# Optimization experiments

Hardware: AMD Instinct MI355X
Metric: run time of the kernel (lower is better)

## Reference

```python
import jax, jax.numpy as jnp
import numpy as np

NC = 512  # n_clusters (symbol alphabet size)
# (kernel, stride, padding) for each of the 17 symbolic conv layers
CFGS = [(7, 4, 0), (3, 1, 1), (3, 1, 1), (3, 1, 1), (3, 1, 1), (3, 2, 1),
        (3, 1, 1), (3, 1, 1), (3, 1, 1), (3, 2, 1), (3, 1, 1), (3, 1, 1),
        (3, 1, 1), (3, 2, 1), (3, 1, 1), (3, 1, 1), (3, 1, 1)]
RELU_AFTER = {0, 1, 3, 5, 7, 9, 11, 13, 15}
INS = [3, 64, 64, 64, 64, 64, 128, 128, 128, 128, 256, 256, 256, 256, 512, 512, 512]
OUTS = [64, 64, 64, 64, 64, 128, 128, 128, 128, 256, 256, 256, 256, 512, 512, 512, 512]


def setup_inputs() -> dict:
    key = jax.random.key(0)
    ks = jax.random.split(key, 26)
    inp = {"x": jax.random.normal(ks[0], (8, 3, 67, 67), dtype=jnp.float32)}
    for i in range(17):
        k = CFGS[i][0]
        inp[f"w{i}"] = jax.random.randint(ks[1 + i], (k * k * INS[i], OUTS[i]), 0, NC, dtype=jnp.int32)
    inp["conv_lut"] = jax.random.randint(ks[18], (NC, NC), 0, NC, dtype=jnp.int32)
    inp["add_lut"] = jax.random.randint(ks[19], (NC, NC), 0, NC, dtype=jnp.int32)
    inp["relu_lut"] = jax.random.randint(ks[20], (NC,), 0, NC, dtype=jnp.int32)
    inp["centroid_lut"] = jnp.sort(jax.random.normal(ks[21], (NC,), dtype=jnp.float32))
    inp["fc_w"] = jax.random.normal(ks[22], (1000, 512), dtype=jnp.float32) * 0.02
    inp["fc_b"] = jnp.zeros((1000,), dtype=jnp.float32)
    return inp


def _extract_patches(s, k, st):
    H, W, C = s.shape
    oh = (H - k) // st + 1
    ow = (W - k) // st + 1
    ri = (jnp.arange(oh) * st)[:, None] + jnp.arange(k)[None, :]  # (oh, k)
    ci = (jnp.arange(ow) * st)[:, None] + jnp.arange(k)[None, :]  # (ow, k)
    p = s[ri][:, :, ci]                      # (oh, k, ow, k, C)
    p = p.transpose(0, 2, 1, 3, 4)           # (oh, ow, k, k, C)
    return p.reshape(oh * ow, k * k * C), oh, ow


def _sym_conv(s, W, conv_lut, add_lut, k, st, pad):
    # LUT-based symbolic convolution: gather product symbols then fold the
    # window with the (non-associative) add_lut, exactly like functools.reduce.
    if pad:
        s = jnp.pad(s, ((pad, pad), (pad, pad), (0, 0)))
    pat, oh, ow = _extract_patches(s, k, st)
    m = conv_lut[pat[:, :, None], W[None, :, :]]
    def step(carry, row):                              # sequential LUT reduce over syms
        return add_lut[carry, row], None
    out, _ = jax.lax.scan(step, m[:, 0, :], jnp.moveaxis(m[:, 1:, :], 1, 0))
    return out.reshape(oh, ow, -1)


def reference(x, w0, w1, w2, w3, w4, w5, w6, w7, w8, w9, w10, w11, w12, w13,
              w14, w15, w16, conv_lut, add_lut, relu_lut, centroid_lut, fc_w, fc_b):
    ws = [w0, w1, w2, w3, w4, w5, w6, w7, w8, w9, w10, w11, w12, w13, w14, w15, w16]

    def per_image(img):                                 # img: (3, 67, 67)
        p = img.transpose(1, 2, 0)                      # (67, 67, 3)
        # discretize: nearest-centroid symbol per scalar (patch_size = 1x1)
        s = jnp.argmin((p[..., None] - centroid_lut) ** 2, axis=-1).astype(jnp.int32)
        for i, (k, st, pad) in enumerate(CFGS):
            s = _sym_conv(s, ws[i], conv_lut, add_lut, k, st, pad)
            if i in RELU_AFTER:
                s = relu_lut[s]
        vals = centroid_lut[s]                          # symbolic_to_image: (2, 2, 512)
        return jnp.mean(vals, axis=(0, 1))              # AdaptiveAvgPool2d((1,1)) -> (512,)

    feats = jax.vmap(per_image)(x)                      # (B, 512)
    return feats @ fc_w.T + fc_b                        # classifier: (B, 1000)
```

## Files before the change

### kernel.cpp

```cpp
#include <hip/hip_runtime.h>

typedef unsigned short u16;

#define NSYM 512

__global__ void build_tables_kernel(const int* __restrict__ conv_i,
                                    const int* __restrict__ add_i,
                                    const int* __restrict__ relu_i,
                                    u16* __restrict__ conv_u,
                                    u16* __restrict__ add_u,
                                    u16* __restrict__ addrelu_u) {
    int i = blockIdx.x * blockDim.x + threadIdx.x;
    if (i < NSYM * NSYM) {
        conv_u[i] = (u16)conv_i[i];
        int a = add_i[i];
        add_u[i] = (u16)a;
        addrelu_u[i] = (u16)relu_i[a];
    }
}

__global__ void quantize_kernel(const float* __restrict__ x,
                                u16* __restrict__ s0,
                                const float* __restrict__ cent,
                                int n) {
    __shared__ float c[NSYM];
    for (int t = threadIdx.x; t < NSYM; t += blockDim.x) c[t] = cent[t];
    __syncthreads();
    int i = blockIdx.x * blockDim.x + threadIdx.x;
    if (i >= n) return;
    int ch = i % 3; int t2 = i / 3; int xx = t2 % 67; int t3 = t2 / 67;
    int y = t3 % 67; int img = t3 / 67;
    float v = x[((img * 3 + ch) * 67 + y) * 67 + xx];
    int lo = 0, hi = NSYM;
    while (lo < hi) { int mid = (lo + hi) >> 1; if (c[mid] < v) lo = mid + 1; else hi = mid; }
    int idx;
    if (lo == 0) idx = 0;
    else if (lo == NSYM) idx = NSYM - 1;
    else {
        float d1 = v - c[lo - 1];
        float d2 = v - c[lo];
        idx = (d1 * d1 <= d2 * d2) ? (lo - 1) : lo;
    }
    s0[i] = (u16)idx;
}

__global__ __launch_bounds__(64) void symconv_kernel(
                               const u16* __restrict__ in, u16* __restrict__ out,
                               const int* __restrict__ Wl,
                               const u16* __restrict__ conv,
                               const u16* __restrict__ addt,
                               const u16* __restrict__ addlast,
                               int H, int Wd, int C, int OC, int nOCG,
                               int K, int ST, int PAD, int OH, int OW) {
    extern __shared__ u16 patch[];
    int bid = blockIdx.x;
    int ocg = bid % nOCG;
    int pix = bid / nOCG;
    int img = pix / (OH * OW);
    int rem = pix - img * (OH * OW);
    int oy = rem / OW;
    int ox = rem - oy * OW;
    int J = K * K * C;
    for (int t = threadIdx.x; t < J; t += 64) {
        int c = t % C; int tt = t / C; int kc = tt % K; int kr = tt / K;
        int iy = oy * ST + kr - PAD;
        int ix = ox * ST + kc - PAD;
        u16 v = 0;
        if (iy >= 0 && iy < H && ix >= 0 && ix < Wd)
            v = in[((img * H + iy) * Wd + ix) * C + c];
        patch[t] = v;
    }
    __syncthreads();
    int oc = ocg * 64 + threadIdx.x;

#define GM(j) ((int)conv[((int)patch[(j)] << 9) + Wl[(j) * OC + oc]])

    int carry = GM(0);
    int mA = GM(1);
    int mB = GM(2);
    int mC = GM(3);
    for (int j = 1; j < J - 3; ++j) {
        int mcur = mA; mA = mB; mB = mC;
        mC = GM(j + 3);
        carry = (int)addt[(carry << 9) + mcur];
    }
    carry = (int)addt[(carry << 9) + mA];
    carry = (int)addt[(carry << 9) + mB];
    carry = (int)addlast[(carry << 9) + mC];
    out[pix * OC + oc] = (u16)carry;
#undef GM
}

__global__ void head_kernel(const u16* __restrict__ s,
                            const float* __restrict__ cent,
                            const float* __restrict__ fcw,
                            const float* __restrict__ fcb,
                            float* __restrict__ out) {
    __shared__ float feats[NSYM];
    int img = blockIdx.x;
    const u16* sp = s + img * 4 * NSYM;
    for (int c = threadIdx.x; c < NSYM; c += blockDim.x) {
        float acc = cent[sp[c]] + cent[sp[NSYM + c]] +
                    cent[sp[2 * NSYM + c]] + cent[sp[3 * NSYM + c]];
        feats[c] = acc * 0.25f;
    }
    __syncthreads();
    int o = blockIdx.y * blockDim.x + threadIdx.x;
    if (o < 1000) {
        float acc = fcb[o];
        const float* wr = fcw + o * NSYM;
        for (int c2 = 0; c2 < NSYM; ++c2) acc += feats[c2] * wr[c2];
        out[img * 1000 + o] = acc;
    }
}

extern "C" void kernel_launch(void* const* d_in, const int* in_sizes, int n_in,
                              void* d_out, int out_size, void* d_ws, size_t ws_size,
                              hipStream_t stream) {
    const float* x = (const float*)d_in[0];
    const int* w[17];
    for (int i = 0; i < 17; ++i) w[i] = (const int*)d_in[1 + i];
    const int* conv_i = (const int*)d_in[18];
    const int* add_i  = (const int*)d_in[19];
    const int* relu_i = (const int*)d_in[20];
    const float* cent = (const float*)d_in[21];
    const float* fcw  = (const float*)d_in[22];
    const float* fcb  = (const float*)d_in[23];
    float* out = (float*)d_out;

    char* p = (char*)d_ws;
    u16* conv_u    = (u16*)p; p += NSYM * NSYM * 2;
    u16* add_u     = (u16*)p; p += NSYM * NSYM * 2;
    u16* addrelu_u = (u16*)p; p += NSYM * NSYM * 2;
    u16* act0      = (u16*)p; p += ((8 * 67 * 67 * 3 * 2 + 255) / 256) * 256;
    u16* actA      = (u16*)p; p += 8 * 16 * 16 * 64 * 2;
    u16* actB      = (u16*)p; p += 8 * 16 * 16 * 64 * 2;

    build_tables_kernel<<<(NSYM * NSYM + 255) / 256, 256, 0, stream>>>(
        conv_i, add_i, relu_i, conv_u, add_u, addrelu_u);

    int nq = 8 * 67 * 67 * 3;
    quantize_kernel<<<(nq + 255) / 256, 256, 0, stream>>>(x, act0, cent, nq);

    struct LC { int K, ST, PAD, C, OC, H, OH, relu; };
    static const LC L[17] = {
        {7,4,0,  3, 64,67,16,1},
        {3,1,1, 64, 64,16,16,1},
        {3,1,1, 64, 64,16,16,0},
        {3,1,1, 64, 64,16,16,1},
        {3,1,1, 64, 64,16,16,0},
        {3,2,1, 64,128,16, 8,1},
        {3,1,1,128,128, 8, 8,0},
        {3,1,1,128,128, 8, 8,1},
        {3,1,1,128,128, 8, 8,0},
        {3,2,1,128,256, 8, 4,1},
        {3,1,1,256,256, 4, 4,0},
        {3,1,1,256,256, 4, 4,1},
        {3,1,1,256,256, 4, 4,0},
        {3,2,1,256,512, 4, 2,1},
        {3,1,1,512,512, 2, 2,0},
        {3,1,1,512,512, 2, 2,1},
        {3,1,1,512,512, 2, 2,0},
    };

    const u16* cur = act0;
    u16* nxt = actA;
    for (int i = 0; i < 17; ++i) {
        int OH = L[i].OH, OW = L[i].OH;
        int nOCG = L[i].OC / 64;
        int grid = 8 * OH * OW * nOCG;
        int J = L[i].K * L[i].K * L[i].C;
        symconv_kernel<<<grid, 64, J * 2, stream>>>(
            cur, nxt, w[i], conv_u, add_u, L[i].relu ? addrelu_u : add_u,
            L[i].H, L[i].H, L[i].C, L[i].OC, nOCG,
            L[i].K, L[i].ST, L[i].PAD, OH, OW);
        cur = nxt;
        nxt = (nxt == actA) ? actB : actA;
    }

    head_kernel<<<dim3(8, 4), 256, 0, stream>>>(cur, cent, fcw, fcb, out);
}
```

Measured before the change: 6.376 ms.

## Split symconv into producer and consumer waves with double-buffered LDS chunks

Each block now runs two waves. One wave gathers conv-LUT product symbols for the next chunk of the window into a swizzled LDS buffer, while the other wave runs the serial add-LUT fold over the current chunk. The aim is to hide the gather latency (weight load plus conv table lookup) behind the dependent add chain. This costs twice the threads per block, extra LDS per block, and a block-wide barrier after every chunk.

```diff
diff --git a/kernel.cpp b/kernel.cpp
--- a/kernel.cpp
+++ b/kernel.cpp
@@ -1,6 +1,7 @@
 #include <hip/hip_runtime.h>
 
 typedef unsigned short u16;
+typedef __attribute__((ext_vector_type(8))) short short8;
 
 #define NSYM 512
 
@@ -44,15 +45,21 @@
     s0[i] = (u16)idx;
 }
 
-__global__ __launch_bounds__(64) void symconv_kernel(
-                               const u16* __restrict__ in, u16* __restrict__ out,
-                               const int* __restrict__ Wl,
-                               const u16* __restrict__ conv,
-                               const u16* __restrict__ addt,
-                               const u16* __restrict__ addlast,
-                               int H, int Wd, int C, int OC, int nOCG,
-                               int K, int ST, int PAD, int OH, int OW) {
-    extern __shared__ u16 patch[];
+__global__ __launch_bounds__(128) void symconv_kernel(
+        const u16* __restrict__ in, u16* __restrict__ out,
+        const int* __restrict__ Wl,
+        const u16* __restrict__ conv,
+        const u16* __restrict__ addt,
+        const u16* __restrict__ addlast,
+        int H, int Wd, int C, int OC, int nOCG,
+        int K, int ST, int PAD, int OH, int OW, int CH) {
+    extern __shared__ char lds[];
+    int J = K * K * C;
+    u16* patch = (u16*)lds;
+    int patchBytes = (J * 2 + 127) & ~127;
+    char* mbuf0 = lds + patchBytes;
+    char* mbuf1 = mbuf0 + CH * 64 * 2;
+
     int bid = blockIdx.x;
     int ocg = bid % nOCG;
     int pix = bid / nOCG;
@@ -60,8 +67,8 @@
     int rem = pix - img * (OH * OW);
     int oy = rem / OW;
     int ox = rem - oy * OW;
-    int J = K * K * C;
-    for (int t = threadIdx.x; t < J; t += 64) {
+
+    for (int t = threadIdx.x; t < J; t += 128) {
         int c = t % C; int tt = t / C; int kc = tt % K; int kr = tt / K;
         int iy = oy * ST + kr - PAD;
         int ix = ox * ST + kc - PAD;
@@ -71,24 +78,95 @@
         patch[t] = v;
     }
     __syncthreads();
-    int oc = ocg * 64 + threadIdx.x;
-
-#define GM(j) ((int)conv[((int)patch[(j)] << 9) + Wl[(j) * OC + oc]])
-
-    int carry = GM(0);
-    int mA = GM(1);
-    int mB = GM(2);
-    int mC = GM(3);
-    for (int j = 1; j < J - 3; ++j) {
-        int mcur = mA; mA = mB; mB = mC;
-        mC = GM(j + 3);
-        carry = (int)addt[(carry << 9) + mcur];
-    }
-    carry = (int)addt[(carry << 9) + mA];
-    carry = (int)addt[(carry << 9) + mB];
-    carry = (int)addlast[(carry << 9) + mC];
-    out[pix * OC + oc] = (u16)carry;
-#undef GM
+
+    int wave = threadIdx.x >> 6;
+    int lane = threadIdx.x & 63;
+    int oc = ocg * 64 + lane;
+    int nch = (J + CH - 1) / CH;
+    int rowbase = lane * CH * 2;
+    int lsw = lane & 7;
+
+    auto produce = [&](int t) {
+        char* dst = (t & 1) ? mbuf1 : mbuf0;
+        int j0 = t * CH;
+        int n = min(CH, J - j0);
+        int nfull = n >> 3, tail = n & 7;
+        for (int g = 0; g < nfull; ++g) {
+            u16 v[8];
+            #pragma unroll
+            for (int u = 0; u < 8; ++u) {
+                int j = j0 + g * 8 + u;
+                int wv = Wl[j * OC + oc];
+                v[u] = conv[((int)patch[j] << 9) + wv];
+            }
+            short8 pk;
+            #pragma unroll
+            for (int u = 0; u < 8; ++u) pk[u] = (short)v[u];
+            *(short8*)(dst + rowbase + ((g ^ lsw) << 4)) = pk;
+        }
+        for (int u = 0; u < tail; ++u) {
+            int j = j0 + nfull * 8 + u;
+            int wv = Wl[j * OC + oc];
+            u16 vv = conv[((int)patch[j] << 9) + wv];
+            *(u16*)(dst + rowbase + ((nfull ^ lsw) << 4) + (u << 1)) = vv;
+        }
+    };
+
+    int carry = 0;
+
+    auto chain = [&](int t) {
+        const char* src = (t & 1) ? mbuf1 : mbuf0;
+        int j0 = t * CH;
+        int n = min(CH, J - j0);
+        bool lastchunk = (j0 + n == J);
+        int ncha = n - (lastchunk ? 1 : 0);
+        int nfull = ncha >> 3, tail = ncha & 7;
+        short8 cur, nxt;
+        int g = 0;
+        if (nfull > 0) {
+            cur = *(const short8*)(src + rowbase + ((0 ^ lsw) << 4));
+            if (t == 0) {
+                if (nfull > 1) nxt = *(const short8*)(src + rowbase + ((1 ^ lsw) << 4));
+                carry = (int)(unsigned short)cur[0];
+                #pragma unroll
+                for (int u = 1; u < 8; ++u)
+                    carry = (int)addt[(carry << 9) + (int)(unsigned short)cur[u]];
+                cur = nxt;
+                g = 1;
+            }
+        }
+        for (; g < nfull; ++g) {
+            if (g + 1 < nfull)
+                nxt = *(const short8*)(src + rowbase + (((g + 1) ^ lsw) << 4));
+            #pragma unroll
+            for (int u = 0; u < 8; ++u)
+                carry = (int)addt[(carry << 9) + (int)(unsigned short)cur[u]];
+            cur = nxt;
+        }
+        for (int u = 0; u < tail; ++u) {
+            int jj = nfull * 8 + u;
+            int m = (int)*(const u16*)(src + rowbase + (((jj >> 3) ^ lsw) << 4) + ((jj & 7) << 1));
+            if (t == 0 && jj == 0) carry = m;
+            else carry = (int)addt[(carry << 9) + m];
+        }
+        if (lastchunk) {
+            int jj = n - 1;
+            int m = (int)*(const u16*)(src + rowbase + (((jj >> 3) ^ lsw) << 4) + ((jj & 7) << 1));
+            carry = (int)addlast[(carry << 9) + m];
+        }
+    };
+
+    if (wave == 1) produce(0);
+    __syncthreads();
+    for (int t = 0; t < nch; ++t) {
+        if (wave == 1) {
+            if (t + 1 < nch) produce(t + 1);
+        } else {
+            chain(t);
+        }
+        __syncthreads();
+    }
+    if (wave == 0) out[pix * OC + oc] = (u16)carry;
 }
 
 __global__ void head_kernel(const u16* __restrict__ s,
@@ -162,6 +240,8 @@
         {3,1,1,512,512, 2, 2,1},
         {3,1,1,512,512, 2, 2,0},
     };
+    static const int CHs[17] = {64, 64,64,64,64, 128, 128,128,128,
+                                192, 192,192,192, 192, 192,192,192};
 
     const u16* cur = act0;
     u16* nxt = actA;
@@ -170,10 +250,13 @@
         int nOCG = L[i].OC / 64;
         int grid = 8 * OH * OW * nOCG;
         int J = L[i].K * L[i].K * L[i].C;
-        symconv_kernel<<<grid, 64, J * 2, stream>>>(
+        int CH = CHs[i];
+        int patchBytes = (J * 2 + 127) & ~127;
+        int ldsBytes = patchBytes + CH * 256;
+        symconv_kernel<<<grid, 128, ldsBytes, stream>>>(
             cur, nxt, w[i], conv_u, add_u, L[i].relu ? addrelu_u : add_u,
             L[i].H, L[i].H, L[i].C, L[i].OC, nOCG,
-            L[i].K, L[i].ST, L[i].PAD, OH, OW);
+            L[i].K, L[i].ST, L[i].PAD, OH, OW, CH);
         cur = nxt;
         nxt = (nxt == actA) ? actB : actA;
     }
```

New measurement: 6.499 ms. About the same (+1.9%).

## Stage weight slice in LDS and share it across several pixels per block

Applied to the files above, without the earlier changes.

Adds a kernel variant that loads the 64-output-channel weight slice for a layer into shared memory as u16, then runs PPB waves, one pixel each, that reuse it. The goal is to cut repeated global int32 weight loads, which the old one-pixel-per-block kernel issued per pixel. Early layers (up to layer 9) use the new path and deeper layers keep the original per-pixel kernel. The cost is much larger LDS use per block (up to about 147KB for layer 9), which lowers occupancy, and a raised dynamic shared memory limit.

```diff
diff --git a/kernel.cpp b/kernel.cpp
--- a/kernel.cpp
+++ b/kernel.cpp
@@ -44,14 +44,76 @@
     s0[i] = (u16)idx;
 }
 
-__global__ __launch_bounds__(64) void symconv_kernel(
-                               const u16* __restrict__ in, u16* __restrict__ out,
-                               const int* __restrict__ Wl,
-                               const u16* __restrict__ conv,
-                               const u16* __restrict__ addt,
-                               const u16* __restrict__ addlast,
-                               int H, int Wd, int C, int OC, int nOCG,
-                               int K, int ST, int PAD, int OH, int OW) {
+__global__ __launch_bounds__(512) void symconv_ldsw_kernel(
+        const u16* __restrict__ in, u16* __restrict__ out,
+        const int* __restrict__ Wl,
+        const u16* __restrict__ conv,
+        const u16* __restrict__ addt,
+        const u16* __restrict__ addlast,
+        int H, int C, int OC, int nOCG,
+        int K, int ST, int PAD, int OH, int OW, int PPB) {
+    extern __shared__ u16 lds[];
+    int J = K * K * C;
+    u16* wlds = lds;
+    u16* patch = lds + J * 64;
+
+    int bid = blockIdx.x;
+    int ocg = bid % nOCG;
+    int pblk = bid / nOCG;
+    int pixel0 = pblk * PPB;
+    int tid = threadIdx.x;
+    int nthr = PPB << 6;
+
+    for (int t = tid; t < J * 64; t += nthr) {
+        int j = t >> 6; int ocp = t & 63;
+        wlds[t] = (u16)Wl[j * OC + (ocg << 6) + ocp];
+    }
+    for (int t = tid; t < PPB * J; t += nthr) {
+        int p = t / J; int j = t - p * J;
+        int c = j % C; int tt = j / C; int kc = tt % K; int kr = tt / K;
+        int pix = pixel0 + p;
+        int img = pix / (OH * OW); int rem = pix - img * (OH * OW);
+        int oy = rem / OW; int ox = rem - oy * OW;
+        int iy = oy * ST + kr - PAD;
+        int ix = ox * ST + kc - PAD;
+        u16 v = 0;
+        if (iy >= 0 && iy < H && ix >= 0 && ix < H)
+            v = in[((img * H + iy) * H + ix) * C + c];
+        patch[p * J + j] = v;
+    }
+    __syncthreads();
+
+    int wave = tid >> 6;
+    int lane = tid & 63;
+    int pix = pixel0 + wave;
+    const u16* pat = patch + wave * J;
+
+#define GM(j) ((int)conv[((int)pat[(j)] << 9) + (int)wlds[((j) << 6) + lane]])
+
+    int carry = GM(0);
+    int mA = GM(1);
+    int mB = GM(2);
+    int mC = GM(3);
+    for (int j = 1; j < J - 3; ++j) {
+        int mcur = mA; mA = mB; mB = mC;
+        mC = GM(j + 3);
+        carry = (int)addt[(carry << 9) + mcur];
+    }
+    carry = (int)addt[(carry << 9) + mA];
+    carry = (int)addt[(carry << 9) + mB];
+    carry = (int)addlast[(carry << 9) + mC];
+    out[pix * OC + (ocg << 6) + lane] = (u16)carry;
+#undef GM
+}
+
+__global__ __launch_bounds__(64) void symconv_glob_kernel(
+        const u16* __restrict__ in, u16* __restrict__ out,
+        const int* __restrict__ Wl,
+        const u16* __restrict__ conv,
+        const u16* __restrict__ addt,
+        const u16* __restrict__ addlast,
+        int H, int C, int OC, int nOCG,
+        int K, int ST, int PAD, int OH, int OW) {
     extern __shared__ u16 patch[];
     int bid = blockIdx.x;
     int ocg = bid % nOCG;
@@ -66,12 +128,12 @@
         int iy = oy * ST + kr - PAD;
         int ix = ox * ST + kc - PAD;
         u16 v = 0;
-        if (iy >= 0 && iy < H && ix >= 0 && ix < Wd)
-            v = in[((img * H + iy) * Wd + ix) * C + c];
+        if (iy >= 0 && iy < H && ix >= 0 && ix < H)
+            v = in[((img * H + iy) * H + ix) * C + c];
         patch[t] = v;
     }
     __syncthreads();
-    int oc = ocg * 64 + threadIdx.x;
+    int oc = (ocg << 6) + threadIdx.x;
 
 #define GM(j) ((int)conv[((int)patch[(j)] << 9) + Wl[(j) * OC + oc]])
 
@@ -142,38 +204,61 @@
     int nq = 8 * 67 * 67 * 3;
     quantize_kernel<<<(nq + 255) / 256, 256, 0, stream>>>(x, act0, cent, nq);
 
-    struct LC { int K, ST, PAD, C, OC, H, OH, relu; };
+    struct LC { int K, ST, PAD, C, OC, H, OH, relu, PPB; };
     static const LC L[17] = {
-        {7,4,0,  3, 64,67,16,1},
-        {3,1,1, 64, 64,16,16,1},
-        {3,1,1, 64, 64,16,16,0},
-        {3,1,1, 64, 64,16,16,1},
-        {3,1,1, 64, 64,16,16,0},
-        {3,2,1, 64,128,16, 8,1},
-        {3,1,1,128,128, 8, 8,0},
-        {3,1,1,128,128, 8, 8,1},
-        {3,1,1,128,128, 8, 8,0},
-        {3,2,1,128,256, 8, 4,1},
-        {3,1,1,256,256, 4, 4,0},
-        {3,1,1,256,256, 4, 4,1},
-        {3,1,1,256,256, 4, 4,0},
-        {3,2,1,256,512, 4, 2,1},
-        {3,1,1,512,512, 2, 2,0},
-        {3,1,1,512,512, 2, 2,1},
-        {3,1,1,512,512, 2, 2,0},
+        {7,4,0,  3, 64,67,16,1, 8},
+        {3,1,1, 64, 64,16,16,1, 8},
+        {3,1,1, 64, 64,16,16,0, 8},
+        {3,1,1, 64, 64,16,16,1, 8},
+        {3,1,1, 64, 64,16,16,0, 8},
+        {3,2,1, 64,128,16, 8,1, 4},
+        {3,1,1,128,128, 8, 8,0, 4},
+        {3,1,1,128,128, 8, 8,1, 4},
+        {3,1,1,128,128, 8, 8,0, 4},
+        {3,2,1,128,256, 8, 4,1, 2},
+        {3,1,1,256,256, 4, 4,0, 0},
+        {3,1,1,256,256, 4, 4,1, 0},
+        {3,1,1,256,256, 4, 4,0, 0},
+        {3,2,1,256,512, 4, 2,1, 0},
+        {3,1,1,512,512, 2, 2,0, 0},
+        {3,1,1,512,512, 2, 2,1, 0},
+        {3,1,1,512,512, 2, 2,0, 0},
     };
+
+    int maxlds = 0;
+    for (int i = 0; i < 17; ++i) {
+        if (L[i].PPB > 0) {
+            int J = L[i].K * L[i].K * L[i].C;
+            int b = J * 64 * 2 + L[i].PPB * J * 2;
+            if (b > maxlds) maxlds = b;
+        }
+    }
+    hipFuncSetAttribute((const void*)symconv_ldsw_kernel,
+                        hipFuncAttributeMaxDynamicSharedMemorySize, maxlds);
 
     const u16* cur = act0;
     u16* nxt = actA;
     for (int i = 0; i < 17; ++i) {
-        int OH = L[i].OH, OW = L[i].OH;
+        int OH = L[i].OH;
         int nOCG = L[i].OC / 64;
-        int grid = 8 * OH * OW * nOCG;
         int J = L[i].K * L[i].K * L[i].C;
-        symconv_kernel<<<grid, 64, J * 2, stream>>>(
-            cur, nxt, w[i], conv_u, add_u, L[i].relu ? addrelu_u : add_u,
-            L[i].H, L[i].H, L[i].C, L[i].OC, nOCG,
-            L[i].K, L[i].ST, L[i].PAD, OH, OW);
+        const u16* lastt = L[i].relu ? addrelu_u : add_u;
+        if (L[i].PPB > 0) {
+            int PPB = L[i].PPB;
+            int pixels = 8 * OH * OH;
+            int grid = (pixels / PPB) * nOCG;
+            int ldsB = J * 64 * 2 + PPB * J * 2;
+            symconv_ldsw_kernel<<<grid, PPB * 64, ldsB, stream>>>(
+                cur, nxt, w[i], conv_u, add_u, lastt,
+                L[i].H, L[i].C, L[i].OC, nOCG,
+                L[i].K, L[i].ST, L[i].PAD, OH, OH, PPB);
+        } else {
+            int grid = 8 * OH * OH * nOCG;
+            symconv_glob_kernel<<<grid, 64, J * 2, stream>>>(
+                cur, nxt, w[i], conv_u, add_u, lastt,
+                L[i].H, L[i].C, L[i].OC, nOCG,
+                L[i].K, L[i].ST, L[i].PAD, OH, OH);
+        }
         cur = nxt;
         nxt = (nxt == actA) ? actB : actA;
     }
```

After: 6.661 ms. +4.5%, slower.
